# Optimization experiments

Measured on AMD Instinct MI355X. Metric: run time of the kernel, lower is better.

## Reference

```python
import jax, jax.numpy as jnp
import numpy as np

N = 200000      # active voxels
CIN = 96        # in_channels == out_channels (identity residual path)
CMID = 192      # max(in,out) * channel_multiplier
OFF = 27        # kernel_size**3 offsets
EPS = 1e-5      # BatchNorm eps


def setup_inputs() -> dict:
    key = jax.random.key(0)
    ks = jax.random.split(key, 6)
    x = jax.random.normal(ks[0], (N, CIN), jnp.float32)
    idx = jax.random.randint(ks[1], (OFF, N), 0, N, jnp.int32)
    mask = jax.random.randint(ks[2], (OFF, N), 0, 2, jnp.int32)
    W1 = jax.random.normal(ks[3], (OFF, CIN, CMID), jnp.float32) / np.float32(np.sqrt(OFF * CIN))
    W2 = jax.random.normal(ks[4], (OFF, CMID, CIN), jnp.float32) / np.float32(np.sqrt(OFF * CMID))
    g1 = jnp.ones((CMID,), jnp.float32)
    b1 = jnp.zeros((CMID,), jnp.float32)
    g2 = jnp.ones((CIN,), jnp.float32)
    b2 = jnp.zeros((CIN,), jnp.float32)
    return {"x": x, "idx": idx, "mask": mask, "W1": W1, "g1": g1, "b1": b1,
            "W2": W2, "g2": g2, "b2": b2}


def _sparse_conv(x, idx, mask, W):
    """Explicit-GEMM sparse conv: per-offset gather -> GEMM -> accumulate.
    x: [N, Cin], idx/mask: [OFF, N], W: [OFF, Cin, Cout] -> [N, Cout]."""
    n = x.shape[0]
    cout = W.shape[-1]

    def body(acc, off):
        i, m, w = off
        g = jnp.where(m[:, None] > 0, x[i], jnp.zeros((), x.dtype))  # gather [N, Cin]
        return acc + g @ w, None

    out, _ = jax.lax.scan(body, jnp.zeros((n, cout), x.dtype), (idx, mask, W))
    return out


def _bn(x, gamma, beta):
    # BatchNorm1d in training mode: batch statistics over the voxel dim.
    mu = jnp.mean(x, axis=0)
    var = jnp.var(x, axis=0)
    return gamma * (x - mu) * jax.lax.rsqrt(var + EPS) + beta


def reference(x, idx, mask, W1, g1, b1, W2, g2, b2):
    h = jax.nn.relu(_bn(_sparse_conv(x, idx, mask, W1), g1, b1))
    h = _bn(_sparse_conv(h, idx, mask, W2), g2, b2)
    return jax.nn.relu(h + x)  # identity residual (in_channels == out_channels)
```

## Files before the change

kernel.cpp:

```cpp
#include <hip/hip_runtime.h>
#include <hip/hip_bf16.h>

typedef unsigned short u16;
typedef __attribute__((ext_vector_type(8))) short short8;
typedef __attribute__((ext_vector_type(4))) float f32x4;
typedef __attribute__((ext_vector_type(8))) unsigned short ushort8v;

#define NVOX 200000
#define NVP  200064
#define NOFF 27
#define NBLK 1563

__device__ __forceinline__ u16 f2bf(float f) {
    __hip_bfloat16 h = __float2bfloat16(f);
    return *reinterpret_cast<u16*>(&h);
}
__device__ __forceinline__ float bf2f(u16 u) {
    union { unsigned int i; float f; } v;
    v.i = ((unsigned int)u) << 16;
    return v.f;
}

#define GLOAD_LDS16(g, l)                                                     \
    __builtin_amdgcn_global_load_lds(                                         \
        (const __attribute__((address_space(1))) unsigned int*)(g),           \
        (__attribute__((address_space(3))) unsigned int*)(l), 16, 0, 0)

__global__ __launch_bounds__(256) void prep_kernel(
    const float* __restrict__ x, const float* __restrict__ W1,
    const float* __restrict__ W2, u16* __restrict__ xb,
    u16* __restrict__ w1t, u16* __restrict__ w2t, float* __restrict__ zbuf)
{
    const int XV = NVOX * 96 / 4;
    const int WC = 62208;
    int t = blockIdx.x * 256 + threadIdx.x;
    if (blockIdx.x == 0 && threadIdx.x < 64) zbuf[threadIdx.x] = 0.f;
    if (t < XV) {
        float4 v = *(const float4*)(x + (size_t)t * 4);
        ushort4 o;
        o.x = f2bf(v.x); o.y = f2bf(v.y); o.z = f2bf(v.z); o.w = f2bf(v.w);
        *(ushort4*)(xb + (size_t)t * 4) = o;
    } else if (t < XV + WC) {
        int j = t - XV;
        int lane = j & 63, rest = j >> 6;
        int nco = rest % 12, rest2 = rest / 12;
        int ks = rest2 % 3, off = rest2 / 3;
        int co = nco * 16 + (lane & 15);
        int kb = ks * 32 + (lane >> 4) * 8;
        const float* src = W1 + (size_t)off * 18432 + (size_t)kb * 192 + co;
        ushort8v ov;
#pragma unroll
        for (int jj = 0; jj < 8; ++jj) ov[jj] = f2bf(src[(size_t)jj * 192]);
        *(ushort8v*)(w1t + (size_t)j * 8) = ov;
    } else if (t < XV + 2 * WC) {
        int j = t - XV - WC;
        int lane = j & 63, rest = j >> 6;
        int nco = rest % 6, rest2 = rest / 6;
        int kk = rest2 % 6, off = rest2 / 6;
        int co = nco * 16 + (lane & 15);
        int kb = kk * 32 + (lane >> 4) * 8;
        const float* src = W2 + (size_t)off * 18432 + (size_t)kb * 96 + co;
        ushort8v ov;
#pragma unroll
        for (int jj = 0; jj < 8; ++jj) ov[jj] = f2bf(src[(size_t)jj * 96]);
        *(ushort8v*)(w2t + (size_t)j * 8) = ov;
    }
}

__global__ __launch_bounds__(256) void lsrc_kernel(
    const int* __restrict__ idxp, const int* __restrict__ mskp,
    int* __restrict__ lsrcG)
{
    int r = blockIdx.x * 256 + threadIdx.x;
    int o = blockIdx.y;
    if (r < NVP) {
        int v = -1;
        if (r < NVOX) {
            if (mskp[(size_t)o * NVOX + r] > 0) v = idxp[(size_t)o * NVOX + r];
        }
        lsrcG[(size_t)o * NVP + r] = v;
    }
}

template<int COUT, int WN, int HFDIV, int MINW>
__global__ __launch_bounds__(512, MINW) void conv_mfma(
    const u16* __restrict__ xb, const int* __restrict__ lsrcG,
    const u16* __restrict__ Wt, const float* __restrict__ zbuf,
    u16* __restrict__ hout, float* __restrict__ part)
{
    constexpr int CIN  = 96 * HFDIV;
    constexpr int WM   = 8 / WN;
    constexpr int FM   = 128 / (WM * 16);
    constexpr int FN   = COUT / (WN * 16);
    constexpr int NCO  = COUT / 16;
    constexpr int SG   = NOFF * HFDIV;
    constexpr int BUFU = 12 * 128 * 8;

    __shared__ u16 ldsA[2 * BUFU];

    const int tid  = threadIdx.x;
    const int row0 = blockIdx.x * 128;
    const int lane = tid & 63;
    const int wid  = tid >> 6;
    const int wm   = wid / WN;
    const int wn   = wid % WN;
    const int lr   = lane & 15;
    const int lk   = lane >> 4;

    const int rStage = tid & 127;
    const int c0 = tid >> 7;
    const int ldsWaveBase = (tid & ~63) * 8;

    int rdBase[FM];
#pragma unroll
    for (int m = 0; m < FM; ++m) {
        int r = wm * (FM * 16) + m * 16 + lr;
        rdBase[m] = r * 8 + lk * 1024;
    }
    const u16* wtw = Wt + (size_t)(wn * FN) * 512 + (size_t)lane * 8;

    f32x4 acc[FM][FN];
#pragma unroll
    for (int m = 0; m < FM; ++m)
#pragma unroll
        for (int n = 0; n < FN; ++n)
            acc[m][n] = (f32x4){0.f, 0.f, 0.f, 0.f};

    auto issueA = [&](int s, int bufSel) {
        int offIdx = (HFDIV == 1) ? s : (s >> 1);
        int hf     = (HFDIV == 1) ? 0 : (s & 1);
        int sv = lsrcG[(size_t)offIdx * NVP + row0 + rStage];
        const u16* g = (sv >= 0)
            ? (xb + (size_t)sv * CIN + hf * 96 + c0 * 8)
            : ((const u16*)zbuf + c0 * 8);
#pragma unroll
        for (int it = 0; it < 3; ++it)
            GLOAD_LDS16(g + it * 32,
                        ldsA + bufSel * BUFU + it * 4096 + ldsWaveBase);
    };

    issueA(0, 0);
    __syncthreads();

    short8 wreg[3][FN];
    int bufSel = 0;
#pragma unroll 1
    for (int s = 0; s < SG; ++s) {
#pragma unroll
        for (int ks = 0; ks < 3; ++ks)
#pragma unroll
            for (int n = 0; n < FN; ++n)
                wreg[ks][n] = *(const short8*)(
                    wtw + ((size_t)(3 * s + ks) * NCO + n) * 512);
        __builtin_amdgcn_sched_barrier(0);
        if (s + 1 < SG) issueA(s + 1, bufSel ^ 1);
        __builtin_amdgcn_sched_barrier(0);
        const u16* abuf = ldsA + bufSel * BUFU;
#pragma unroll
        for (int ks = 0; ks < 3; ++ks) {
#pragma unroll
            for (int m = 0; m < FM; ++m) {
                short8 af = *(const short8*)(abuf + rdBase[m] + ks * 4096);
#pragma unroll
                for (int n = 0; n < FN; ++n)
                    acc[m][n] = __builtin_amdgcn_mfma_f32_16x16x32_bf16(
                        af, wreg[ks][n], acc[m][n], 0, 0, 0);
            }
        }
        __syncthreads();
        bufSel ^= 1;
    }

    float* smf = (float*)ldsA;
#pragma unroll
    for (int n = 0; n < FN; ++n) {
        float s1 = 0.f, s2 = 0.f;
#pragma unroll
        for (int m = 0; m < FM; ++m)
#pragma unroll
            for (int q = 0; q < 4; ++q) {
                float v = acc[m][n][q];
                s1 += v; s2 += v * v;
            }
        s1 += __shfl_xor(s1, 16); s1 += __shfl_xor(s1, 32);
        s2 += __shfl_xor(s2, 16); s2 += __shfl_xor(s2, 32);
        if (lane < 16) {
            int col = wn * (FN * 16) + n * 16 + lr;
            smf[(wm * COUT + col) * 2 + 0] = s1;
            smf[(wm * COUT + col) * 2 + 1] = s2;
        }
    }
    __syncthreads();
    if (tid < 2 * COUT) {
        int z = tid / COUT, cc = tid % COUT;
        float v = 0.f;
#pragma unroll
        for (int w = 0; w < WM; ++w) v += smf[(w * COUT + cc) * 2 + z];
        part[(size_t)blockIdx.x * (2 * COUT) + z * COUT + cc] = v;
    }

#pragma unroll
    for (int m = 0; m < FM; ++m) {
#pragma unroll
        for (int q = 0; q < 4; ++q) {
            int row = row0 + wm * (FM * 16) + m * 16 + lk * 4 + q;
            if (row < NVOX) {
#pragma unroll
                for (int n = 0; n < FN; ++n) {
                    int col = wn * (FN * 16) + n * 16 + lr;
                    hout[(size_t)row * COUT + col] = f2bf(acc[m][n][q]);
                }
            }
        }
    }
}

template<int COUT>
__global__ __launch_bounds__(256) void bn_statsB(
    const float* __restrict__ part, const float* __restrict__ g,
    const float* __restrict__ bv, float* __restrict__ ss)
{
    const int c = blockIdx.x;
    const int t = threadIdx.x;
    float s1 = 0.f, s2 = 0.f;
    for (int b = t; b < NBLK; b += 256) {
        s1 += part[(size_t)b * 2 * COUT + c];
        s2 += part[(size_t)b * 2 * COUT + COUT + c];
    }
#pragma unroll
    for (int d = 1; d < 64; d <<= 1) {
        s1 += __shfl_xor(s1, d);
        s2 += __shfl_xor(s2, d);
    }
    __shared__ float rs[8];
    int w = t >> 6;
    if ((t & 63) == 0) { rs[w] = s1; rs[4 + w] = s2; }
    __syncthreads();
    if (t == 0) {
        s1 = rs[0] + rs[1] + rs[2] + rs[3];
        s2 = rs[4] + rs[5] + rs[6] + rs[7];
        float mu  = s1 * (1.0f / NVOX);
        float var = s2 * (1.0f / NVOX) - mu * mu;
        float sc  = g[c] * rsqrtf(var + 1e-5f);
        ss[c] = sc;
        ss[COUT + c] = bv[c] - mu * sc;
    }
}

template<int COUT>
__global__ __launch_bounds__(256) void bn_apply_relu(
    u16* __restrict__ h, const float* __restrict__ ss)
{
    int t = blockIdx.x * 256 + threadIdx.x;
    int c0 = (t * 8) % COUT;
    ushort8v v = *(ushort8v*)(h + (size_t)t * 8);
#pragma unroll
    for (int j = 0; j < 8; ++j) {
        float f = bf2f(v[j]);
        f = fmaxf(f * ss[c0 + j] + ss[COUT + c0 + j], 0.f);
        v[j] = f2bf(f);
    }
    *(ushort8v*)(h + (size_t)t * 8) = v;
}

__global__ __launch_bounds__(256) void final_kernel(
    const u16* __restrict__ h2, const float* __restrict__ x,
    const float* __restrict__ ss, float* __restrict__ out)
{
    int t = blockIdx.x * 256 + threadIdx.x;
    int c0 = (t * 8) % 96;
    ushort8v v = *(const ushort8v*)(h2 + (size_t)t * 8);
    float4 x0 = *(const float4*)(x + (size_t)t * 8);
    float4 x1 = *(const float4*)(x + (size_t)t * 8 + 4);
    float xs[8] = {x0.x, x0.y, x0.z, x0.w, x1.x, x1.y, x1.z, x1.w};
    float o[8];
#pragma unroll
    for (int j = 0; j < 8; ++j) {
        float f = bf2f(v[j]) * ss[c0 + j] + ss[96 + c0 + j] + xs[j];
        o[j] = fmaxf(f, 0.f);
    }
    *(float4*)(out + (size_t)t * 8)     = (float4){o[0], o[1], o[2], o[3]};
    *(float4*)(out + (size_t)t * 8 + 4) = (float4){o[4], o[5], o[6], o[7]};
}

extern "C" void kernel_launch(void* const* d_in, const int* in_sizes, int n_in,
                              void* d_out, int out_size, void* d_ws, size_t ws_size,
                              hipStream_t stream)
{
    const float* x    = (const float*)d_in[0];
    const int*   idx  = (const int*)d_in[1];
    const int*   mask = (const int*)d_in[2];
    const float* W1   = (const float*)d_in[3];
    const float* g1   = (const float*)d_in[4];
    const float* b1   = (const float*)d_in[5];
    const float* W2   = (const float*)d_in[6];
    const float* g2   = (const float*)d_in[7];
    const float* b2   = (const float*)d_in[8];

    unsigned char* ws = (unsigned char*)d_ws;
    u16*  xb    = (u16*)ws;
    u16*  w1t   = (u16*)(ws + 38400000);
    u16*  w2t   = (u16*)(ws + 39395328);
    u16*  h2    = (u16*)(ws + 40390656);
    float* part = (float*)(ws + 78790656);
    float* ss1  = (float*)(ws + 81191424);
    float* ss2  = (float*)(ws + 81192960);
    float* zbuf = (float*)(ws + 81193728);
    int*  lsrcG = (int*)(ws + 81193984);

    u16* h = (u16*)d_out;

    prep_kernel<<<19236, 256, 0, stream>>>(x, W1, W2, xb, w1t, w2t, zbuf);
    lsrc_kernel<<<dim3(782, 27), 256, 0, stream>>>(idx, mask, lsrcG);

    conv_mfma<192, 4, 1, 4><<<NBLK, 512, 0, stream>>>(xb, lsrcG, w1t, zbuf, h, part);
    bn_statsB<192><<<192, 256, 0, stream>>>(part, g1, b1, ss1);
    bn_apply_relu<192><<<18750, 256, 0, stream>>>(h, ss1);

    conv_mfma<96, 2, 2, 6><<<NBLK, 512, 0, stream>>>(h, lsrcG, w2t, zbuf, h2, part);
    bn_statsB<96><<<96, 256, 0, stream>>>(part, g2, b2, ss2);
    final_kernel<<<9375, 256, 0, stream>>>(h2, x, ss2, (float*)d_out);
}
```

Baseline: 752.8 us.

## Deepen conv gather pipeline to three LDS stages with register-double-buffered weights

Moves the sparse-conv MFMA kernel from a two-buffer to a three-buffer LDS ring, so the gather for step s+2 is issued while step s computes. It also prefetches the neighbour-index values two steps ahead and double-buffers the weight fragments in registers. Full __syncthreads inside the loop become raw s_barriers, with one explicit vmcnt wait in the prologue. The aim is to hide gather latency, at the cost of more LDS and registers per block. The second conv's min-waves hint drops from 6 to 4, which lowers occupancy, and the loop relies on the compiler to wait for in-flight LDS-DMA loads before each barrier.

```diff
diff --git a/kernel.cpp b/kernel.cpp
--- a/kernel.cpp
+++ b/kernel.cpp
@@ -82,8 +82,8 @@
     }
 }
 
-template<int COUT, int WN, int HFDIV, int MINW>
-__global__ __launch_bounds__(512, MINW) void conv_mfma(
+template<int COUT, int WN, int HFDIV>
+__global__ __launch_bounds__(512, 4) void conv_mfma(
     const u16* __restrict__ xb, const int* __restrict__ lsrcG,
     const u16* __restrict__ Wt, const float* __restrict__ zbuf,
     u16* __restrict__ hout, float* __restrict__ part)
@@ -96,7 +96,7 @@
     constexpr int SG   = NOFF * HFDIV;
     constexpr int BUFU = 12 * 128 * 8;
 
-    __shared__ u16 ldsA[2 * BUFU];
+    __shared__ u16 ldsA[3 * BUFU];
 
     const int tid  = threadIdx.x;
     const int row0 = blockIdx.x * 128;
@@ -126,36 +126,54 @@
         for (int n = 0; n < FN; ++n)
             acc[m][n] = (f32x4){0.f, 0.f, 0.f, 0.f};
 
-    auto issueA = [&](int s, int bufSel) {
+    auto hfOf = [&](int s) -> int { return (HFDIV == 1) ? 0 : (s & 1); };
+    auto loadSv = [&](int s) -> int {
         int offIdx = (HFDIV == 1) ? s : (s >> 1);
-        int hf     = (HFDIV == 1) ? 0 : (s & 1);
-        int sv = lsrcG[(size_t)offIdx * NVP + row0 + rStage];
+        return lsrcG[(size_t)offIdx * NVP + row0 + rStage];
+    };
+    auto gatherTo = [&](int sv, int hf, int bsel) {
         const u16* g = (sv >= 0)
             ? (xb + (size_t)sv * CIN + hf * 96 + c0 * 8)
             : ((const u16*)zbuf + c0 * 8);
 #pragma unroll
         for (int it = 0; it < 3; ++it)
             GLOAD_LDS16(g + it * 32,
-                        ldsA + bufSel * BUFU + it * 4096 + ldsWaveBase);
+                        ldsA + bsel * BUFU + it * 4096 + ldsWaveBase);
     };
-
-    issueA(0, 0);
-    __syncthreads();
-
-    short8 wreg[3][FN];
-    int bufSel = 0;
-#pragma unroll 1
-    for (int s = 0; s < SG; ++s) {
+    auto loadW = [&](int s, short8 (&w)[3][FN]) {
 #pragma unroll
         for (int ks = 0; ks < 3; ++ks)
 #pragma unroll
             for (int n = 0; n < FN; ++n)
-                wreg[ks][n] = *(const short8*)(
+                w[ks][n] = *(const short8*)(
                     wtw + ((size_t)(3 * s + ks) * NCO + n) * 512);
+    };
+
+    short8 wA[3][FN], wB[3][FN];
+    int svA, svB;
+
+    {
+        int sv0 = loadSv(0);
+        gatherTo(sv0, hfOf(0), 0);
+        int sv1 = loadSv(1);
+        gatherTo(sv1, hfOf(1), 1);
+        loadW(0, wA);
+        svA = loadSv(2);
+        svB = loadSv(3);
+        asm volatile("s_waitcnt vmcnt(14)" ::: "memory");
+        __builtin_amdgcn_s_barrier();
         __builtin_amdgcn_sched_barrier(0);
-        if (s + 1 < SG) issueA(s + 1, bufSel ^ 1);
+    }
+
+    auto stepBody = [&](int s, short8 (&wcur)[3][FN], short8 (&wnxt)[3][FN],
+                        int bsel) {
+        int bsel2 = (bsel >= 1) ? bsel - 1 : bsel + 2;
+        if (s + 2 < SG) gatherTo(svA, hfOf(s + 2), bsel2);
+        svA = svB;
+        if (s + 4 < SG) svB = loadSv(s + 4);
+        if (s + 1 < SG) loadW(s + 1, wnxt);
         __builtin_amdgcn_sched_barrier(0);
-        const u16* abuf = ldsA + bufSel * BUFU;
+        const u16* abuf = ldsA + bsel * BUFU;
 #pragma unroll
         for (int ks = 0; ks < 3; ++ks) {
 #pragma unroll
@@ -164,13 +182,22 @@
 #pragma unroll
                 for (int n = 0; n < FN; ++n)
                     acc[m][n] = __builtin_amdgcn_mfma_f32_16x16x32_bf16(
-                        af, wreg[ks][n], acc[m][n], 0, 0, 0);
+                        af, wcur[ks][n], acc[m][n], 0, 0, 0);
             }
         }
-        __syncthreads();
-        bufSel ^= 1;
-    }
-
+        __builtin_amdgcn_s_barrier();
+        __builtin_amdgcn_sched_barrier(0);
+    };
+
+    int sel = 0, s = 0;
+#pragma unroll 1
+    for (; s + 1 < SG; s += 2) {
+        stepBody(s,     wA, wB, sel); sel = (sel == 2) ? 0 : sel + 1;
+        stepBody(s + 1, wB, wA, sel); sel = (sel == 2) ? 0 : sel + 1;
+    }
+    if (s < SG) stepBody(s, wA, wB, sel);
+
+    __syncthreads();
     float* smf = (float*)ldsA;
 #pragma unroll
     for (int n = 0; n < FN; ++n) {
@@ -313,11 +340,11 @@
     prep_kernel<<<19236, 256, 0, stream>>>(x, W1, W2, xb, w1t, w2t, zbuf);
     lsrc_kernel<<<dim3(782, 27), 256, 0, stream>>>(idx, mask, lsrcG);
 
-    conv_mfma<192, 4, 1, 4><<<NBLK, 512, 0, stream>>>(xb, lsrcG, w1t, zbuf, h, part);
+    conv_mfma<192, 4, 1><<<NBLK, 512, 0, stream>>>(xb, lsrcG, w1t, zbuf, h, part);
     bn_statsB<192><<<192, 256, 0, stream>>>(part, g1, b1, ss1);
     bn_apply_relu<192><<<18750, 256, 0, stream>>>(h, ss1);
 
-    conv_mfma<96, 2, 2, 6><<<NBLK, 512, 0, stream>>>(h, lsrcG, w2t, zbuf, h2, part);
+    conv_mfma<96, 2, 2><<<NBLK, 512, 0, stream>>>(h, lsrcG, w2t, zbuf, h2, part);
     bn_statsB<96><<<96, 256, 0, stream>>>(part, g2, b2, ss2);
     final_kernel<<<9375, 256, 0, stream>>>(h2, x, ss2, (float*)d_out);
 }
```

New measurement: 815.6 us. 1.08x slower.

## Replace direct global-to-LDS gathers with register-staged triple-buffered pipeline

Applied to the files above, without the earlier changes.

The gather of input rows no longer uses global_load_lds. Each thread loads a 16-byte chunk into registers, prefetching the index two stages ahead and the data one stage ahead, and writes it to LDS midway through the MFMA work. LDS is now triple-buffered, and a rotated, padded plane layout is meant to avoid bank conflicts. The aim is to hide gather latency behind compute and keep the single barrier per stage. In exchange it uses more VGPRs, and the second conv's occupancy hint drops from 6 to 4 waves.

```diff
diff --git a/kernel.cpp b/kernel.cpp
--- a/kernel.cpp
+++ b/kernel.cpp
@@ -20,11 +20,6 @@
     v.i = ((unsigned int)u) << 16;
     return v.f;
 }
-
-#define GLOAD_LDS16(g, l)                                                     \
-    __builtin_amdgcn_global_load_lds(                                         \
-        (const __attribute__((address_space(1))) unsigned int*)(g),           \
-        (__attribute__((address_space(3))) unsigned int*)(l), 16, 0, 0)
 
 __global__ __launch_bounds__(256) void prep_kernel(
     const float* __restrict__ x, const float* __restrict__ W1,
@@ -82,8 +77,8 @@
     }
 }
 
-template<int COUT, int WN, int HFDIV, int MINW>
-__global__ __launch_bounds__(512, MINW) void conv_mfma(
+template<int COUT, int WN, int HFDIV>
+__global__ __launch_bounds__(512, 4) void conv_mfma(
     const u16* __restrict__ xb, const int* __restrict__ lsrcG,
     const u16* __restrict__ Wt, const float* __restrict__ zbuf,
     u16* __restrict__ hout, float* __restrict__ part)
@@ -94,9 +89,10 @@
     constexpr int FN   = COUT / (WN * 16);
     constexpr int NCO  = COUT / 16;
     constexpr int SG   = NOFF * HFDIV;
-    constexpr int BUFU = 12 * 128 * 8;
-
-    __shared__ u16 ldsA[2 * BUFU];
+    constexpr int PLN  = 520;
+    constexpr int BUFD = 12 * PLN;
+
+    __shared__ unsigned int ldsA[3 * BUFD];
 
     const int tid  = threadIdx.x;
     const int row0 = blockIdx.x * 128;
@@ -107,15 +103,22 @@
     const int lr   = lane & 15;
     const int lk   = lane >> 4;
 
-    const int rStage = tid & 127;
-    const int c0 = tid >> 7;
-    const int ldsWaveBase = (tid & ~63) * 8;
-
-    int rdBase[FM];
+    int svOff[3], aOffU[3], wDw[3];
+#pragma unroll
+    for (int it = 0; it < 3; ++it) {
+        int l = it * 512 + tid;
+        int r = l / 12, c = l % 12;
+        svOff[it] = row0 + r;
+        aOffU[it] = c * 8;
+        int p = (c + r) % 12;
+        wDw[it] = p * PLN + r * 4;
+    }
+    int rB4[FM], rm12[FM];
 #pragma unroll
     for (int m = 0; m < FM; ++m) {
         int r = wm * (FM * 16) + m * 16 + lr;
-        rdBase[m] = r * 8 + lk * 1024;
+        rB4[m]  = r * 4;
+        rm12[m] = (lk + r) % 12;
     }
     const u16* wtw = Wt + (size_t)(wn * FN) * 512 + (size_t)lane * 8;
 
@@ -126,51 +129,81 @@
         for (int n = 0; n < FN; ++n)
             acc[m][n] = (f32x4){0.f, 0.f, 0.f, 0.f};
 
-    auto issueA = [&](int s, int bufSel) {
+    int sv[3];
+    uint4 ar[3];
+    auto svLoad = [&](int s) {
         int offIdx = (HFDIV == 1) ? s : (s >> 1);
-        int hf     = (HFDIV == 1) ? 0 : (s & 1);
-        int sv = lsrcG[(size_t)offIdx * NVP + row0 + rStage];
-        const u16* g = (sv >= 0)
-            ? (xb + (size_t)sv * CIN + hf * 96 + c0 * 8)
-            : ((const u16*)zbuf + c0 * 8);
+        const int* base = lsrcG + (size_t)offIdx * NVP;
+#pragma unroll
+        for (int it = 0; it < 3; ++it) sv[it] = base[svOff[it]];
+    };
+    auto aIssue = [&](int s) {
+        int hf = (HFDIV == 1) ? 0 : (s & 1);
+#pragma unroll
+        for (int it = 0; it < 3; ++it) {
+            const u16* g = (sv[it] >= 0)
+                ? (xb + (size_t)sv[it] * CIN + hf * 96 + aOffU[it])
+                : ((const u16*)zbuf + aOffU[it]);
+            ar[it] = *(const uint4*)g;
+        }
+    };
+    auto aWrite = [&](int bsel) {
+        unsigned int* b = ldsA + bsel * BUFD;
 #pragma unroll
         for (int it = 0; it < 3; ++it)
-            GLOAD_LDS16(g + it * 32,
-                        ldsA + bufSel * BUFU + it * 4096 + ldsWaveBase);
-    };
-
-    issueA(0, 0);
-    __syncthreads();
+            *(uint4*)(b + wDw[it]) = ar[it];
+    };
 
     short8 wreg[3][FN];
-    int bufSel = 0;
-#pragma unroll 1
-    for (int s = 0; s < SG; ++s) {
+    auto loadW = [&](int s) {
 #pragma unroll
         for (int ks = 0; ks < 3; ++ks)
 #pragma unroll
             for (int n = 0; n < FN; ++n)
                 wreg[ks][n] = *(const short8*)(
                     wtw + ((size_t)(3 * s + ks) * NCO + n) * 512);
-        __builtin_amdgcn_sched_barrier(0);
-        if (s + 1 < SG) issueA(s + 1, bufSel ^ 1);
-        __builtin_amdgcn_sched_barrier(0);
-        const u16* abuf = ldsA + bufSel * BUFU;
-#pragma unroll
-        for (int ks = 0; ks < 3; ++ks) {
-#pragma unroll
-            for (int m = 0; m < FM; ++m) {
-                short8 af = *(const short8*)(abuf + rdBase[m] + ks * 4096);
-#pragma unroll
-                for (int n = 0; n < FN; ++n)
-                    acc[m][n] = __builtin_amdgcn_mfma_f32_16x16x32_bf16(
-                        af, wreg[ks][n], acc[m][n], 0, 0, 0);
-            }
-        }
-        __syncthreads();
-        bufSel ^= 1;
-    }
-
+    };
+    auto mfmaKs = [&](int ks, const unsigned int* abuf) {
+#pragma unroll
+        for (int m = 0; m < FM; ++m) {
+            int p = rm12[m] + ks * 4;
+            if (p >= 12) p -= 12;
+            short8 af = *(const short8*)(abuf + p * PLN + rB4[m]);
+#pragma unroll
+            for (int n = 0; n < FN; ++n)
+                acc[m][n] = __builtin_amdgcn_mfma_f32_16x16x32_bf16(
+                    af, wreg[ks][n], acc[m][n], 0, 0, 0);
+        }
+    };
+
+    svLoad(0); aIssue(0); aWrite(0);
+    svLoad(1); aIssue(1); aWrite(1);
+    svLoad(2);
+    __syncthreads();
+
+    int cur = 0, nxt2 = 2;
+#pragma unroll 1
+    for (int s = 0; s < SG; ++s) {
+        loadW(s);
+        __builtin_amdgcn_sched_barrier(0);
+        if (s + 2 < SG) aIssue(s + 2);
+        if (s + 3 < SG) svLoad(s + 3);
+        __builtin_amdgcn_sched_barrier(0);
+        const unsigned int* abuf = ldsA + cur * BUFD;
+        mfmaKs(0, abuf);
+        mfmaKs(1, abuf);
+        __builtin_amdgcn_sched_barrier(0);
+        if (s + 2 < SG) aWrite(nxt2);
+        __builtin_amdgcn_sched_barrier(0);
+        mfmaKs(2, abuf);
+        __builtin_amdgcn_sched_barrier(0);
+        __builtin_amdgcn_s_barrier();
+        __builtin_amdgcn_sched_barrier(0);
+        cur  = (cur == 2)  ? 0 : cur + 1;
+        nxt2 = (nxt2 == 2) ? 0 : nxt2 + 1;
+    }
+
+    __syncthreads();
     float* smf = (float*)ldsA;
 #pragma unroll
     for (int n = 0; n < FN; ++n) {
@@ -313,11 +346,11 @@
     prep_kernel<<<19236, 256, 0, stream>>>(x, W1, W2, xb, w1t, w2t, zbuf);
     lsrc_kernel<<<dim3(782, 27), 256, 0, stream>>>(idx, mask, lsrcG);
 
-    conv_mfma<192, 4, 1, 4><<<NBLK, 512, 0, stream>>>(xb, lsrcG, w1t, zbuf, h, part);
+    conv_mfma<192, 4, 1><<<NBLK, 512, 0, stream>>>(xb, lsrcG, w1t, zbuf, h, part);
     bn_statsB<192><<<192, 256, 0, stream>>>(part, g1, b1, ss1);
     bn_apply_relu<192><<<18750, 256, 0, stream>>>(h, ss1);
 
-    conv_mfma<96, 2, 2, 6><<<NBLK, 512, 0, stream>>>(h, lsrcG, w2t, zbuf, h2, part);
+    conv_mfma<96, 2, 2><<<NBLK, 512, 0, stream>>>(h, lsrcG, w2t, zbuf, h2, part);
     bn_statsB<96><<<96, 256, 0, stream>>>(part, g2, b2, ss2);
     final_kernel<<<9375, 256, 0, stream>>>(h2, x, ss2, (float*)d_out);
 }
```

Result: slower. 1.630 ms (+116.5%).
